# Performance work log

Hardware: AMD Instinct MI355X
Metric: run time of the kernel (lower is better)

Reference implementation:

```python
import jax, jax.numpy as jnp
import numpy as np

KAPPA = 5.0
EPS_NORM = 1e-12  # torch F.normalize eps
EPS_LOG = 1e-09


def setup_inputs() -> dict:
    key = jax.random.key(0)
    student_output = jax.random.normal(key, (16384, 256), dtype=jnp.float32)
    return {"student_output": student_output}


def reference(student_output) -> jnp.ndarray:
    # L2-normalize rows (matches F.normalize: x / max(||x||, eps))
    norm = jnp.linalg.norm(student_output, axis=-1, keepdims=True)
    x_norm = student_output / jnp.maximum(norm, EPS_NORM)
    # pairwise cosine similarity [n, n]
    sim = x_norm @ x_norm.T
    kernel = jnp.exp(KAPPA * sim)
    density_estimates = kernel.sum(axis=1)  # [n]
    entropy = -jnp.mean(jnp.log(density_estimates + EPS_LOG))
    return entropy
```

## Files before the change

kernel.cpp:

```cpp
#include <hip/hip_runtime.h>


#define NROWS 16384
#define KDIM 256
#define NTILE 128
#define NT (NROWS / NTILE)
#define NSTRIP 4
#define TOTAL_BLOCKS (NT * NSTRIP)

#define SQRT_KLOG2E 2.68579577857f

typedef int i32x4_t __attribute__((ext_vector_type(4)));
typedef int i32x8_t __attribute__((ext_vector_type(8)));
typedef float f32x16_t __attribute__((ext_vector_type(16)));
typedef __attribute__((address_space(1))) const void global_cvoid_t;
typedef __attribute__((address_space(3))) void lds_void_t;

#if __has_builtin(__builtin_amdgcn_exp2f)
#define EXP2(x) __builtin_amdgcn_exp2f(x)
#else
#define EXP2(x) exp2f(x)
#endif

union frag8 { i32x8_t v8; i32x4_t v4[2]; };

__global__ __launch_bounds__(256)
void kde_normalize(const float* __restrict__ X, unsigned int* __restrict__ Xn8,
                   float* __restrict__ density, unsigned int* __restrict__ ticket) {
  const int wave = threadIdx.x >> 6;
  const int lane = threadIdx.x & 63;
  const int row = blockIdx.x * 4 + wave;
  const float4 v = ((const float4*)(X + (size_t)row * KDIM))[lane];
  float ss = v.x * v.x + v.y * v.y + v.z * v.z + v.w * v.w;
  ss += __shfl_xor(ss, 1);
  ss += __shfl_xor(ss, 2);
  ss += __shfl_xor(ss, 4);
  ss += __shfl_xor(ss, 8);
  ss += __shfl_xor(ss, 16);
  ss += __shfl_xor(ss, 32);
  const float scale = SQRT_KLOG2E / fmaxf(sqrtf(ss), 1e-12f);
  int p = 0;
  p = __builtin_amdgcn_cvt_pk_fp8_f32(v.x * scale, v.y * scale, p, false);
  p = __builtin_amdgcn_cvt_pk_fp8_f32(v.z * scale, v.w * scale, p, true);
  Xn8[(size_t)row * 64 + lane] = (unsigned int)p;
  if (threadIdx.x < 4) density[blockIdx.x * 4 + threadIdx.x] = 0.0f;
  if (blockIdx.x == 0 && threadIdx.x == 0) *ticket = 0u;
}

__global__ __launch_bounds__(512, 4)
void kde_gemm(const unsigned char* __restrict__ Xn8, float* __restrict__ density,
              unsigned int* __restrict__ ticket, float* __restrict__ out) {
  extern __shared__ char smem[];
  char* buf0 = smem;
  char* buf1 = smem + 32768;

  const int tid = threadIdx.x;
  const int wave = tid >> 6;
  const int lane = tid & 63;
  const int wr = wave >> 1;
  const int wc = wave & 1;
  const int m32 = lane & 31;
  const int h = lane >> 5;
  const int bi = blockIdx.x;
  const int s = blockIdx.y;
  const int t0 = s * 16;
  const int nt = (s == 0 && bi < NT / 2) ? 17 : 16;
  const char* Xb = (const char*)Xn8;

#define STAGE(base_row, dst)                                                      \
  for (int c = wave; c < 32; c += 8) {                                            \
    const int rt = c >> 3, kb = (c >> 1) & 3, hh = c & 1;                         \
    const size_t gofs =                                                           \
        (size_t)((base_row) + rt * 32 + m32) * KDIM + kb * 64 + h * 32 + hh * 16; \
    __builtin_amdgcn_global_load_lds((global_cvoid_t*)(Xb + gofs),                \
                                     (lds_void_t*)((dst) + c * 1024), 16, 0, 0);  \
  }

  STAGE(bi * NTILE, buf0);
  STAGE(((bi + t0) & (NT - 1)) * NTILE, buf1);
  __syncthreads();

  frag8 areg[4];
#pragma unroll
  for (int kb = 0; kb < 4; kb++) {
    const char* pa = buf0 + (wr * 8 + kb * 2) * 1024 + lane * 16;
    areg[kb].v4[0] = *(const i32x4_t*)pa;
    areg[kb].v4[1] = *(const i32x4_t*)(pa + 1024);
  }
  __syncthreads();

  float rs[16];
#pragma unroll
  for (int r = 0; r < 16; r++) rs[r] = 0.0f;

  for (int k = 0; k < nt; ++k) {
    const int t = t0 + (k == 16 ? 48 : k) + (k == 16 ? 16 : 0);
    const int J = (bi + t) & (NT - 1);
    char* rbuf = (k & 1) ? buf0 : buf1;
    char* sbuf = (k & 1) ? buf1 : buf0;

    if (k + 1 < nt) {
      const int tn = t0 + (k + 1 == 16 ? 64 : k + 1);
      STAGE(((bi + tn) & (NT - 1)) * NTILE, sbuf);
    }

    f32x16_t acc[2];
#pragma unroll
    for (int j = 0; j < 2; j++) acc[j] = (f32x16_t)0.0f;

#pragma unroll
    for (int kb = 0; kb < 4; ++kb) {
      frag8 bf[2];
#pragma unroll
      for (int j = 0; j < 2; j++) {
        const char* pb = rbuf + ((wc * 2 + j) * 8 + kb * 2) * 1024 + lane * 16;
        bf[j].v4[0] = *(const i32x4_t*)pb;
        bf[j].v4[1] = *(const i32x4_t*)(pb + 1024);
      }
#pragma unroll
      for (int j = 0; j < 2; j++)
        acc[j] = __builtin_amdgcn_mfma_scale_f32_32x32x64_f8f6f4(
            areg[kb].v8, bf[j].v8, acc[j], 0, 0, 0, 127, 0, 127);
    }

    float cs[2] = {0.0f, 0.0f};
#pragma unroll
    for (int j = 0; j < 2; j++)
#pragma unroll
      for (int r = 0; r < 16; r++) {
        const float e = EXP2(acc[j][r]);
        rs[r] += e;
        cs[j] += e;
      }

    if (t != 0) {
#pragma unroll
      for (int j = 0; j < 2; j++) {
        float v = cs[j] + __shfl_xor(cs[j], 32);
        if (h == 0)
          atomicAdd(&density[J * NTILE + wc * 64 + j * 32 + m32], v);
      }
    }

    __syncthreads();
  }

#pragma unroll
  for (int r = 0; r < 16; r++) {
    float v = rs[r];
    v += __shfl_xor(v, 1);
    v += __shfl_xor(v, 2);
    v += __shfl_xor(v, 4);
    v += __shfl_xor(v, 8);
    v += __shfl_xor(v, 16);
    if (m32 == 0) {
      const int row = bi * NTILE + wr * 32 + (r & 3) + 8 * (r >> 2) + 4 * h;
      atomicAdd(&density[row], v);
    }
  }
#undef STAGE

  __syncthreads();
  if (tid == 0) {
    __threadfence();
    ((volatile unsigned int*)smem)[0] = atomicAdd(ticket, 1u);
  }
  __syncthreads();
  if (((volatile unsigned int*)smem)[0] == TOTAL_BLOCKS - 1) {
    __threadfence();
    float ssum = 0.0f;
    for (int i = tid; i < NROWS; i += 512) {
      const float d = __hip_atomic_load(&density[i], __ATOMIC_RELAXED,
                                        __HIP_MEMORY_SCOPE_AGENT);
      ssum += logf(d + 1e-9f);
    }
    ssum += __shfl_xor(ssum, 1);
    ssum += __shfl_xor(ssum, 2);
    ssum += __shfl_xor(ssum, 4);
    ssum += __shfl_xor(ssum, 8);
    ssum += __shfl_xor(ssum, 16);
    ssum += __shfl_xor(ssum, 32);
    float* red = ((float*)smem) + 16;
    if (lane == 0) red[wave] = ssum;
    __syncthreads();
    if (tid == 0) {
      float tot = 0.0f;
      for (int w = 0; w < 8; w++) tot += red[w];
      out[0] = -tot / (float)NROWS;
    }
  }
}

extern "C" void kernel_launch(void* const* d_in, const int* in_sizes, int n_in,
                              void* d_out, int out_size, void* d_ws, size_t ws_size,
                              hipStream_t stream) {
  const float* X = (const float*)d_in[0];
  float* out = (float*)d_out;
  char* ws = (char*)d_ws;
  unsigned int* Xn8 = (unsigned int*)ws;
  float* density = (float*)(ws + (size_t)NROWS * KDIM);
  unsigned int* ticket = (unsigned int*)(density + NROWS);

  hipFuncSetAttribute((const void*)kde_gemm,
                      hipFuncAttributeMaxDynamicSharedMemorySize, 65536);

  kde_normalize<<<NROWS / 4, 256, 0, stream>>>(X, Xn8, density, ticket);
  kde_gemm<<<dim3(NT, NSTRIP), 512, 65536, stream>>>((const unsigned char*)ws,
                                                     density, ticket, out);
}
```

Before: 124.7 us.

## Use 4 waves per block with 64x64 per-wave tiles in KDE GEMM

The GEMM block drops from 8 waves to 4, and each wave now computes a 2x2 grid of 32x32 MFMA tiles (64x64) instead of 1x2. Each B fragment read from LDS is reused across two A row tiles, which cuts LDS traffic per MFMA, and exp row sums are kept as float2 pairs. The cost is more accumulator registers per wave and fewer waves to hide latency, and the launch bounds change from (512,4) to (256,2).

Result: slower. 136.6 us (+9.5%).

```diff
diff --git a/kernel.cpp b/kernel.cpp
--- a/kernel.cpp
+++ b/kernel.cpp
@@ -12,6 +12,7 @@
 
 typedef int i32x4_t __attribute__((ext_vector_type(4)));
 typedef int i32x8_t __attribute__((ext_vector_type(8)));
+typedef float f32x2_t __attribute__((ext_vector_type(2)));
 typedef float f32x16_t __attribute__((ext_vector_type(16)));
 typedef __attribute__((address_space(1))) const void global_cvoid_t;
 typedef __attribute__((address_space(3))) void lds_void_t;
@@ -47,7 +48,7 @@
   if (blockIdx.x == 0 && threadIdx.x == 0) *ticket = 0u;
 }
 
-__global__ __launch_bounds__(512, 4)
+__global__ __launch_bounds__(256, 2)
 void kde_gemm(const unsigned char* __restrict__ Xn8, float* __restrict__ density,
               unsigned int* __restrict__ ticket, float* __restrict__ out) {
   extern __shared__ char smem[];
@@ -57,8 +58,8 @@
   const int tid = threadIdx.x;
   const int wave = tid >> 6;
   const int lane = tid & 63;
-  const int wr = wave >> 1;
-  const int wc = wave & 1;
+  const int wr2 = wave >> 1;
+  const int wc2 = wave & 1;
   const int m32 = lane & 31;
   const int h = lane >> 5;
   const int bi = blockIdx.x;
@@ -68,7 +69,7 @@
   const char* Xb = (const char*)Xn8;
 
 #define STAGE(base_row, dst)                                                      \
-  for (int c = wave; c < 32; c += 8) {                                            \
+  for (int c = wave; c < 32; c += 4) {                                            \
     const int rt = c >> 3, kb = (c >> 1) & 3, hh = c & 1;                         \
     const size_t gofs =                                                           \
         (size_t)((base_row) + rt * 32 + m32) * KDIM + kb * 64 + h * 32 + hh * 16; \
@@ -80,84 +81,99 @@
   STAGE(((bi + t0) & (NT - 1)) * NTILE, buf1);
   __syncthreads();
 
-  frag8 areg[4];
-#pragma unroll
-  for (int kb = 0; kb < 4; kb++) {
-    const char* pa = buf0 + (wr * 8 + kb * 2) * 1024 + lane * 16;
-    areg[kb].v4[0] = *(const i32x4_t*)pa;
-    areg[kb].v4[1] = *(const i32x4_t*)(pa + 1024);
-  }
-  __syncthreads();
-
-  float rs[16];
-#pragma unroll
-  for (int r = 0; r < 16; r++) rs[r] = 0.0f;
+  frag8 areg[2][4];
+#pragma unroll
+  for (int rt = 0; rt < 2; rt++)
+#pragma unroll
+    for (int kb = 0; kb < 4; kb++) {
+      const char* pa =
+          buf0 + (((wr2 * 2 + rt) * 8) + kb * 2) * 1024 + lane * 16;
+      areg[rt][kb].v4[0] = *(const i32x4_t*)pa;
+      areg[rt][kb].v4[1] = *(const i32x4_t*)(pa + 1024);
+    }
+  __syncthreads();
+
+  f32x2_t rs2[2][8];
+#pragma unroll
+  for (int rt = 0; rt < 2; rt++)
+#pragma unroll
+    for (int r = 0; r < 8; r++) rs2[rt][r] = (f32x2_t)0.0f;
 
   for (int k = 0; k < nt; ++k) {
-    const int t = t0 + (k == 16 ? 48 : k) + (k == 16 ? 16 : 0);
+    const int t = (k == 16) ? 64 : (t0 + k);
     const int J = (bi + t) & (NT - 1);
     char* rbuf = (k & 1) ? buf0 : buf1;
     char* sbuf = (k & 1) ? buf1 : buf0;
 
     if (k + 1 < nt) {
-      const int tn = t0 + (k + 1 == 16 ? 64 : k + 1);
+      const int tn = (k + 1 == 16) ? 64 : (t0 + k + 1);
       STAGE(((bi + tn) & (NT - 1)) * NTILE, sbuf);
     }
 
-    f32x16_t acc[2];
-#pragma unroll
-    for (int j = 0; j < 2; j++) acc[j] = (f32x16_t)0.0f;
+    f32x16_t acc[2][2];
+#pragma unroll
+    for (int rt = 0; rt < 2; rt++)
+#pragma unroll
+      for (int ct = 0; ct < 2; ct++) acc[rt][ct] = (f32x16_t)0.0f;
 
 #pragma unroll
     for (int kb = 0; kb < 4; ++kb) {
       frag8 bf[2];
 #pragma unroll
-      for (int j = 0; j < 2; j++) {
-        const char* pb = rbuf + ((wc * 2 + j) * 8 + kb * 2) * 1024 + lane * 16;
-        bf[j].v4[0] = *(const i32x4_t*)pb;
-        bf[j].v4[1] = *(const i32x4_t*)(pb + 1024);
+      for (int ct = 0; ct < 2; ct++) {
+        const char* pb =
+            rbuf + (((wc2 * 2 + ct) * 8) + kb * 2) * 1024 + lane * 16;
+        bf[ct].v4[0] = *(const i32x4_t*)pb;
+        bf[ct].v4[1] = *(const i32x4_t*)(pb + 1024);
       }
 #pragma unroll
-      for (int j = 0; j < 2; j++)
-        acc[j] = __builtin_amdgcn_mfma_scale_f32_32x32x64_f8f6f4(
-            areg[kb].v8, bf[j].v8, acc[j], 0, 0, 0, 127, 0, 127);
-    }
-
-    float cs[2] = {0.0f, 0.0f};
-#pragma unroll
-    for (int j = 0; j < 2; j++)
-#pragma unroll
-      for (int r = 0; r < 16; r++) {
-        const float e = EXP2(acc[j][r]);
-        rs[r] += e;
-        cs[j] += e;
+      for (int rt = 0; rt < 2; rt++)
+#pragma unroll
+        for (int ct = 0; ct < 2; ct++)
+          acc[rt][ct] = __builtin_amdgcn_mfma_scale_f32_32x32x64_f8f6f4(
+              areg[rt][kb].v8, bf[ct].v8, acc[rt][ct], 0, 0, 0, 127, 0, 127);
+    }
+
+#pragma unroll
+    for (int ct = 0; ct < 2; ct++) {
+      f32x2_t c2 = (f32x2_t)0.0f;
+#pragma unroll
+      for (int rt = 0; rt < 2; rt++)
+#pragma unroll
+        for (int r2 = 0; r2 < 8; r2++) {
+          f32x2_t e;
+          e.x = EXP2(acc[rt][ct][2 * r2]);
+          e.y = EXP2(acc[rt][ct][2 * r2 + 1]);
+          rs2[rt][r2] += e;
+          c2 += e;
+        }
+      if (t != 0) {
+        float cs = c2.x + c2.y;
+        cs += __shfl_xor(cs, 32);
+        if (h == 0)
+          atomicAdd(&density[J * NTILE + wc2 * 64 + ct * 32 + m32], cs);
       }
-
-    if (t != 0) {
-#pragma unroll
-      for (int j = 0; j < 2; j++) {
-        float v = cs[j] + __shfl_xor(cs[j], 32);
-        if (h == 0)
-          atomicAdd(&density[J * NTILE + wc * 64 + j * 32 + m32], v);
+    }
+
+    __syncthreads();
+  }
+
+#pragma unroll
+  for (int rt = 0; rt < 2; rt++)
+#pragma unroll
+    for (int r = 0; r < 16; r++) {
+      float v = rs2[rt][r >> 1][r & 1];
+      v += __shfl_xor(v, 1);
+      v += __shfl_xor(v, 2);
+      v += __shfl_xor(v, 4);
+      v += __shfl_xor(v, 8);
+      v += __shfl_xor(v, 16);
+      if (m32 == 0) {
+        const int row = bi * NTILE + wr2 * 64 + rt * 32 +
+                        (r & 3) + 8 * (r >> 2) + 4 * h;
+        atomicAdd(&density[row], v);
       }
     }
-
-    __syncthreads();
-  }
-
-#pragma unroll
-  for (int r = 0; r < 16; r++) {
-    float v = rs[r];
-    v += __shfl_xor(v, 1);
-    v += __shfl_xor(v, 2);
-    v += __shfl_xor(v, 4);
-    v += __shfl_xor(v, 8);
-    v += __shfl_xor(v, 16);
-    if (m32 == 0) {
-      const int row = bi * NTILE + wr * 32 + (r & 3) + 8 * (r >> 2) + 4 * h;
-      atomicAdd(&density[row], v);
-    }
-  }
 #undef STAGE
 
   __syncthreads();
@@ -169,7 +185,7 @@
   if (((volatile unsigned int*)smem)[0] == TOTAL_BLOCKS - 1) {
     __threadfence();
     float ssum = 0.0f;
-    for (int i = tid; i < NROWS; i += 512) {
+    for (int i = tid; i < NROWS; i += 256) {
       const float d = __hip_atomic_load(&density[i], __ATOMIC_RELAXED,
                                         __HIP_MEMORY_SCOPE_AGENT);
       ssum += logf(d + 1e-9f);
@@ -185,7 +201,7 @@
     __syncthreads();
     if (tid == 0) {
       float tot = 0.0f;
-      for (int w = 0; w < 8; w++) tot += red[w];
+      for (int w = 0; w < 4; w++) tot += red[w];
       out[0] = -tot / (float)NROWS;
     }
   }
@@ -205,6 +221,6 @@
                       hipFuncAttributeMaxDynamicSharedMemorySize, 65536);
 
   kde_normalize<<<NROWS / 4, 256, 0, stream>>>(X, Xn8, density, ticket);
-  kde_gemm<<<dim3(NT, NSTRIP), 512, 65536, stream>>>((const unsigned char*)ws,
+  kde_gemm<<<dim3(NT, NSTRIP), 256, 65536, stream>>>((const unsigned char*)ws,
                                                      density, ticket, out);
 }
```
